# Optimization experiments

Hardware: AMD Instinct MI355X
Metric: run time of the kernel (lower is better)

Reference implementation:

```python
import jax, jax.numpy as jnp
import numpy as np

D_K = 64
N_STEPS = 4
NEG = -1e9  # stand-in for -inf; keeps vjp NaN-free, numerically identical softmax


def setup_inputs() -> dict:
    key = jax.random.key(0)
    ks = jax.random.split(key, 12)
    B, N, D = 4, 2048, 1024
    s = 0.02
    return {
        "hidden": jax.random.normal(ks[0], (B, N, D), jnp.float32),
        "W1": jax.random.normal(ks[1], (64, D), jnp.float32) * s,
        "b1": jnp.zeros((64,), jnp.float32),
        "W2": jax.random.normal(ks[2], (28, 64), jnp.float32) * s,
        "b2": jnp.zeros((28,), jnp.float32),
        "Wq": jax.random.normal(ks[3], (D_K, 28), jnp.float32) * s,
        "Wk": jax.random.normal(ks[4], (D_K, 28), jnp.float32) * s,
        "Wc": jax.random.normal(ks[5], (1, 28), jnp.float32) * s,
        "bc": jnp.zeros((1,), jnp.float32),
        "Wv": jax.random.normal(ks[6], (D_K, D), jnp.float32) * s,
        "Wo": jax.random.normal(ks[7], (D, D_K), jnp.float32) * s,  # torch inits this to zeros; randomized for a non-trivial baseline
        "step_size": jnp.asarray(0.5, jnp.float32),
        "charge_decay": jnp.asarray(0.3, jnp.float32),
        "layer_idx": 0,
    }


def reference(hidden, W1, b1, W2, b2, Wq, Wk, Wc, bc, Wv, Wo, step_size, charge_decay, layer_idx):
    B, N, D = hidden.shape
    # features come from detached hidden in the torch code
    h_sg = jax.lax.stop_gradient(hidden)
    f = jax.nn.gelu(h_sg @ W1.T + b1, approximate=False)  # [B,N,64]
    features = jax.nn.sigmoid(f @ W2.T + b2)              # [B,N,28]
    Q = features @ Wq.T                                   # [B,N,64]
    K = features @ Wk.T                                   # [B,N,64]
    compat = jnp.einsum('bnd,bmd->bnm', Q, K) / jnp.float32(np.sqrt(D_K))
    charge = jax.nn.sigmoid(features @ Wc.T + bc)[..., 0]  # [B,N]
    causal = jnp.tril(jnp.ones((N, N), dtype=bool))
    logits = jnp.where(causal, compat, NEG)
    for _ in range(N_STEPS):
        attn = jax.nn.softmax(logits, axis=-1)            # [B,N,N]
        received = attn.sum(axis=-2)                      # [B,N]
        charge = charge * (1.0 - charge_decay * jax.nn.sigmoid(received - 1.0))
        energy = -compat * charge[:, :, None] * charge[:, None, :]
        logits = jnp.where(causal, logits - step_size * energy, NEG)
    attn = jax.nn.softmax(logits, axis=-1)
    V = hidden @ Wv.T                                     # [B,N,64]
    out = jnp.einsum('bnm,bmd->bnd', attn, V) @ Wo.T      # [B,N,D]
    return out * 0.1
```

## Files before the change

kernel.cpp:

```cpp
#include <hip/hip_runtime.h>
#include <hip/hip_bf16.h>

typedef unsigned short ushort_t;
typedef short bf16x8 __attribute__((ext_vector_type(8)));
typedef ushort_t u16x8 __attribute__((ext_vector_type(8)));
typedef float f32x4 __attribute__((ext_vector_type(4)));

#define DEV static __device__ __forceinline__

DEV float bf2f(ushort_t u) { unsigned v = ((unsigned)u) << 16; float f; __builtin_memcpy(&f, &v, 4); return f; }
DEV short f2bf(float x) { __hip_bfloat16 h = __float2bfloat16(x); short s; __builtin_memcpy(&s, &h, 2); return s; }
DEV float sigm(float x) { return 1.0f / (1.0f + __expf(-x)); }

DEV bf16x8 cvt8(float4 a0, float4 a1) {
    bf16x8 t;
    t[0] = f2bf(a0.x); t[1] = f2bf(a0.y); t[2] = f2bf(a0.z); t[3] = f2bf(a0.w);
    t[4] = f2bf(a1.x); t[5] = f2bf(a1.y); t[6] = f2bf(a1.z); t[7] = f2bf(a1.w);
    return t;
}
DEV bf16x8 ld8f(const float* __restrict__ p) {
    return cvt8(*reinterpret_cast<const float4*>(p), *reinterpret_cast<const float4*>(p + 4));
}

__global__ __launch_bounds__(256, 3) void k_fv(const float* __restrict__ h,
        const float* __restrict__ W1, const float* __restrict__ Wv,
        float* __restrict__ FVp) {
    int bid = blockIdx.x;
    int kh = bid & 1;
    int m0 = (bid >> 1) * 16;
    int wave = threadIdx.x >> 6, lane = threadIdx.x & 63;
    int l16 = lane & 15, quad = lane >> 4;
    const float* B = (wave < 2) ? W1 : Wv;
    int cb = (wave & 1) * 32;
    f32x4 acc[2] = {};
    const float* arow = h + (long)(m0 + l16) * 1024 + kh * 512;
    const float* brow0 = B + (long)(cb + l16) * 1024 + kh * 512;
    const float* brow1 = B + (long)(cb + 16 + l16) * 1024 + kh * 512;
    for (int kc = 0; kc < 512; kc += 128) {
        float4 ra[4][2], r0[4][2], r1[4][2];
#pragma unroll
        for (int u = 0; u < 4; u++) {
            int ko = kc + u * 32 + quad * 8;
            ra[u][0] = *reinterpret_cast<const float4*>(arow + ko);
            ra[u][1] = *reinterpret_cast<const float4*>(arow + ko + 4);
            r0[u][0] = *reinterpret_cast<const float4*>(brow0 + ko);
            r0[u][1] = *reinterpret_cast<const float4*>(brow0 + ko + 4);
            r1[u][0] = *reinterpret_cast<const float4*>(brow1 + ko);
            r1[u][1] = *reinterpret_cast<const float4*>(brow1 + ko + 4);
        }
#pragma unroll
        for (int u = 0; u < 4; u++) {
            bf16x8 af = cvt8(ra[u][0], ra[u][1]);
            bf16x8 b0 = cvt8(r0[u][0], r0[u][1]);
            bf16x8 b1v = cvt8(r1[u][0], r1[u][1]);
            acc[0] = __builtin_amdgcn_mfma_f32_16x16x32_bf16(af, b0, acc[0], 0, 0, 0);
            acc[1] = __builtin_amdgcn_mfma_f32_16x16x32_bf16(af, b1v, acc[1], 0, 0, 0);
        }
    }
    int colbase = ((wave >= 2) ? 64 : 0) + cb;
    float* outp = FVp + (long)kh * 8192 * 128;
#pragma unroll
    for (int c = 0; c < 2; c++)
#pragma unroll
        for (int rr = 0; rr < 4; rr++) {
            int row = m0 + quad * 4 + rr;
            outp[(long)row * 128 + colbase + c * 16 + l16] = acc[c][rr];
        }
}

__global__ __launch_bounds__(256) void k_vbt(const float* __restrict__ FVp, ushort_t* __restrict__ VbT) {
    __shared__ float tL[64][65];
    int r0 = blockIdx.x * 64;
    for (int i = threadIdx.x; i < 64 * 64; i += 256) {
        int r = i >> 6, d = i & 63;
        long idx = (long)(r0 + r) * 128 + 64 + d;
        tL[r][d] = FVp[idx] + FVp[8192L * 128 + idx];
    }
    __syncthreads();
    for (int i = threadIdx.x; i < 64 * 64; i += 256) {
        int d = i >> 6, r = i & 63;
        VbT[(long)d * 8192 + r0 + r] = (ushort_t)f2bf(tL[r][d]);
    }
}

__global__ __launch_bounds__(256) void k_feat(const float* __restrict__ FVp,
        const float* __restrict__ b1, const float* __restrict__ W2, const float* __restrict__ b2,
        const float* __restrict__ Wq, const float* __restrict__ Wk,
        const float* __restrict__ Wc, const float* __restrict__ bc,
        ushort_t* __restrict__ Qb, ushort_t* __restrict__ Kb,
        float* __restrict__ charge0, float* __restrict__ received) {
    __shared__ float w2L[28 * 65], wqL[64 * 29], wkL[64 * 29], wcL[28], b2L[28];
    __shared__ float fL[4][64], featL[4][28];
    int tid = threadIdx.x;
    for (int i = tid; i < 28 * 64; i += 256) w2L[(i >> 6) * 65 + (i & 63)] = W2[i];
    for (int i = tid; i < 64 * 28; i += 256) {
        int r = i / 28, c = i - r * 28;
        wqL[r * 29 + c] = Wq[i];
        wkL[r * 29 + c] = Wk[i];
    }
    if (tid < 28) { wcL[tid] = Wc[tid]; b2L[tid] = b2[tid]; }
    __syncthreads();
    int w = tid >> 6, lane = tid & 63;
    float b1v = b1[lane];
    float bcv = bc[0];
    for (int it = 0; it < 8; it++) {
        int row = blockIdx.x * 32 + it * 4 + w;
        long idx = (long)row * 128 + lane;
        float x = FVp[idx] + FVp[8192L * 128 + idx] + b1v;
        fL[w][lane] = 0.5f * x * (1.0f + erff(x * 0.70710678118654752f));
        __syncthreads();
        if (lane < 28) {
            float s = b2L[lane];
#pragma unroll
            for (int j = 0; j < 64; j++) s += fL[w][j] * w2L[lane * 65 + j];
            featL[w][lane] = sigm(s);
        }
        __syncthreads();
        float q = 0.f, k = 0.f;
#pragma unroll
        for (int i = 0; i < 28; i++) {
            float fv = featL[w][i];
            q += fv * wqL[lane * 29 + i];
            k += fv * wkL[lane * 29 + i];
        }
        Qb[row * 64 + lane] = (ushort_t)f2bf(q * 0.125f);
        Kb[row * 64 + lane] = (ushort_t)f2bf(k);
        if (lane == 0) {
            float c = bcv;
#pragma unroll
            for (int i = 0; i < 28; i++) c += featL[w][i] * wcL[i];
            charge0[row] = sigm(c);
            received[row] = 0.f;
        }
        __syncthreads();
    }
}

DEV void tri_decode(int r, int& ti, int& tj) {
    int t = (int)((sqrtf(8.f * (float)r + 1.f) - 1.f) * 0.5f);
    while ((t + 1) * (t + 2) / 2 <= r) t++;
    while (t * (t + 1) / 2 > r) t--;
    ti = t;
    tj = r - t * (t + 1) / 2;
}

__global__ __launch_bounds__(256) void k_compat(const ushort_t* __restrict__ Qb,
                                                const ushort_t* __restrict__ Kb,
                                                ushort_t* __restrict__ compat) {
    int bid = blockIdx.x;
    int b = bid / 136, r = bid % 136, ti, tj;
    tri_decode(r, ti, tj);
    int wave = threadIdx.x >> 6, lane = threadIdx.x & 63;
    int l16 = lane & 15, quad = lane >> 4;
    int rbase = b * 2048 + ti * 128 + wave * 32;
    int cbase = b * 2048 + tj * 128;
    f32x4 acc[2][8] = {};
#pragma unroll
    for (int kc = 0; kc < 64; kc += 32) {
        int ko = kc + quad * 8;
        bf16x8 af[2], bf[8];
#pragma unroll
        for (int f = 0; f < 2; f++) af[f] = *reinterpret_cast<const bf16x8*>(Qb + (long)(rbase + f * 16 + l16) * 64 + ko);
#pragma unroll
        for (int f = 0; f < 8; f++) bf[f] = *reinterpret_cast<const bf16x8*>(Kb + (long)(cbase + f * 16 + l16) * 64 + ko);
#pragma unroll
        for (int i = 0; i < 2; i++)
#pragma unroll
            for (int j = 0; j < 8; j++)
                acc[i][j] = __builtin_amdgcn_mfma_f32_16x16x32_bf16(af[i], bf[j], acc[i][j], 0, 0, 0);
    }
    int colt = tj * 128;
#pragma unroll
    for (int i = 0; i < 2; i++)
#pragma unroll
        for (int j = 0; j < 8; j++)
#pragma unroll
            for (int rr = 0; rr < 4; rr++) {
                long rowg = rbase + i * 16 + quad * 4 + rr;
                int col = colt + j * 16 + l16;
                compat[rowg * 2048 + col] = (ushort_t)f2bf(acc[i][j][rr]);
            }
}

template <int T>
__global__ __launch_bounds__(256) void k_rowstats(const ushort_t* __restrict__ compat,
        const float4* __restrict__ charges4, const float* __restrict__ stepp,
        float* __restrict__ Lp) {
    int bid = blockIdx.x;
    int z = bid & 1;
    int b = (bid >> 1) & 3;
    int rt = 127 - (bid >> 3);
    int w = threadIdx.x >> 6, lane = threadIdx.x & 63;
    int rw0 = rt * 16 + w * 4;
    int colbase = b * 2048;
    float step = stepp[0];
    float rfx[4] = {}, rfy[4] = {}, rfz[4] = {}, rfw[4] = {};
    if (T > 0) {
#pragma unroll
        for (int r = 0; r < 4; r++) {
            float4 c4 = charges4[colbase + rw0 + r];
            rfx[r] = step * c4.x;
            if (T > 1) rfy[r] = step * c4.y;
            if (T > 2) rfz[r] = step * c4.z;
            if (T > 3) rfw[r] = step * c4.w;
        }
    }
    const ushort_t* crow0 = compat + (long)(colbase + rw0) * 2048;
    float S[4] = {0.f, 0.f, 0.f, 0.f};
    int nmax = rw0 + 3;
    int mhi = min(nmax, z * 1024 + 1023);
    for (int m = z * 1024 + lane; m <= mhi; m += 64) {
        ushort_t cv[4];
#pragma unroll
        for (int r = 0; r < 4; r++) cv[r] = crow0[(long)r * 2048 + m];
        float sx = 0.f, sy = 0.f, sz = 0.f, sw = 0.f;
        if (T > 0) {
            float4 ch = charges4[colbase + m];
            sx = ch.x; sy = ch.y; sz = ch.z; sw = ch.w;
        }
#pragma unroll
        for (int r = 0; r < 4; r++) {
            float sg = 1.f;
            if (T > 0) sg += rfx[r] * sx;
            if (T > 1) sg += rfy[r] * sy;
            if (T > 2) sg += rfz[r] * sz;
            if (T > 3) sg += rfw[r] * sw;
            float e = (m <= rw0 + r) ? __expf(bf2f(cv[r]) * sg) : 0.f;
            S[r] += e;
        }
    }
#pragma unroll
    for (int off = 32; off > 0; off >>= 1) {
#pragma unroll
        for (int r = 0; r < 4; r++) S[r] += __shfl_down(S[r], off);
    }
    if (lane == 0) {
#pragma unroll
        for (int r = 0; r < 4; r++) Lp[z * 8192 + colbase + rw0 + r] = S[r];
    }
}

template <int T>
__global__ __launch_bounds__(256) void k_colsum(const ushort_t* __restrict__ compat,
        const float4* __restrict__ charges4, const float* __restrict__ stepp,
        const float* __restrict__ Lp, float* __restrict__ received) {
    __shared__ float sums[128];
    __shared__ float nvx[32], nvy[32], nvz[32], nvw[32], nLi[32];
    int bid = blockIdx.x;
    int b = bid / 544, rem = bid % 544;
    int q = rem & 3, r = rem >> 2, ti, tj;
    tri_decode(r, ti, tj);
    int tid = threadIdx.x;
    int ml = tid & 127, half = tid >> 7;
    if (tid < 32) {
        int nid = b * 2048 + ti * 128 + q * 32 + tid;
        nLi[tid] = 1.0f / fmaxf(Lp[nid] + Lp[8192 + nid], 1e-30f);
        if (T > 0) {
            float4 cn = charges4[nid];
            nvx[tid] = cn.x;
            if (T > 1) nvy[tid] = cn.y;
            if (T > 2) nvz[tid] = cn.z;
            if (T > 3) nvw[tid] = cn.w;
        }
    }
    __syncthreads();
    int m = tj * 128 + ml;
    int mid = b * 2048 + m;
    float step = stepp[0];
    float cx = 0.f, cy = 0.f, cz = 0.f, cw = 0.f;
    if (T > 0) {
        float4 cm = charges4[mid];
        cx = step * cm.x;
        if (T > 1) cy = step * cm.y;
        if (T > 2) cz = step * cm.z;
        if (T > 3) cw = step * cm.w;
    }
    float acc = 0.f;
    bool diag = (ti == tj);
    const ushort_t* cbase_p = compat + (long)(b * 2048 + ti * 128 + q * 32) * 2048 + m;
    for (int k = 0; k < 16; k += 4) {
        ushort_t cvv[4];
        int nli[4];
#pragma unroll
        for (int u = 0; u < 4; u++) {
            nli[u] = half + 2 * (k + u);
            cvv[u] = cbase_p[(long)nli[u] * 2048];
        }
#pragma unroll
        for (int u = 0; u < 4; u++) {
            float sg = 1.f;
            if (T > 0) sg += cx * nvx[nli[u]];
            if (T > 1) sg += cy * nvy[nli[u]];
            if (T > 2) sg += cz * nvz[nli[u]];
            if (T > 3) sg += cw * nvw[nli[u]];
            float p = __expf(bf2f(cvv[u]) * sg) * nLi[nli[u]];
            if (!diag || m <= ti * 128 + q * 32 + nli[u]) acc += p;
        }
    }
    if (half == 0) sums[ml] = acc;
    __syncthreads();
    if (half == 1) sums[ml] += acc;
    __syncthreads();
    if (tid < 128) atomicAdd(&received[b * 2048 + tj * 128 + tid], sums[tid]);
}

template <int T>
__global__ void k_charge(float* __restrict__ received, const float* __restrict__ charge0,
                         float4* __restrict__ charges4, const float* __restrict__ decayp) {
    int i = blockIdx.x * 256 + threadIdx.x;
    if (i >= 8192) return;
    float decay = decayp[0];
    float rcv = received[i];
    float sg = 1.0f / (1.0f + __expf(1.0f - rcv));
    float prev = (T == 1) ? charge0[i] : ((const float*)&charges4[i])[T - 2];
    ((float*)&charges4[i])[T - 1] = prev * (1.f - decay * sg);
    received[i] = 0.f;
}

__global__ __launch_bounds__(256) void k_pv(const ushort_t* __restrict__ compat,
        const float4* __restrict__ charges4, const float* __restrict__ stepp,
        const ushort_t* __restrict__ VbT, float* __restrict__ Oacc) {
    __shared__ float accL[3][64][17];
    __shared__ float ssL[4][16];
    int bid = blockIdx.x;
    int b = bid & 3, rtile = 127 - (bid >> 2);
    int r0 = rtile * 16;
    int w = threadIdx.x >> 6, lane = threadIdx.x & 63;
    int l16 = lane & 15, quad = lane >> 4;
    int rowl = r0 + l16;
    int rid = b * 2048 + rowl;
    float step = stepp[0];
    float4 c4 = charges4[rid];
    float rx = step * c4.x, ry = step * c4.y, rz = step * c4.z, rw = step * c4.w;
    const ushort_t* crow = compat + (long)rid * 2048;
    f32x4 acc[4] = {};
    float Ss = 0.f;
    int colend = r0 + 16;
    for (int kc = w * 32; kc < colend; kc += 128) {
        int mk = kc + quad * 8;
        u16x8 cv = *reinterpret_cast<const u16x8*>(crow + mk);
        const float4* chp = charges4 + b * 2048 + mk;
        bf16x8 pf;
#pragma unroll
        for (int j = 0; j < 8; j++) {
            float4 ch = chp[j];
            float sg = 1.f + rx * ch.x + ry * ch.y + rz * ch.z + rw * ch.w;
            float p = (mk + j <= rowl) ? __expf(bf2f(cv[j]) * sg) : 0.f;
            Ss += p;
            pf[j] = f2bf(p);
        }
        bf16x8 vf[4];
#pragma unroll
        for (int f = 0; f < 4; f++)
            vf[f] = *reinterpret_cast<const bf16x8*>(VbT + (long)(f * 16 + l16) * 8192 + b * 2048 + mk);
#pragma unroll
        for (int f = 0; f < 4; f++)
            acc[f] = __builtin_amdgcn_mfma_f32_16x16x32_bf16(pf, vf[f], acc[f], 0, 0, 0);
    }
    Ss += __shfl_xor(Ss, 16);
    Ss += __shfl_xor(Ss, 32);
    if (quad == 0) ssL[w][l16] = Ss;
    if (w > 0) {
#pragma unroll
        for (int f = 0; f < 4; f++)
#pragma unroll
            for (int rr = 0; rr < 4; rr++)
                accL[w - 1][lane][f * 4 + rr] = acc[f][rr];
    }
    __syncthreads();
    if (w == 0) {
#pragma unroll
        for (int f = 0; f < 4; f++)
#pragma unroll
            for (int rr = 0; rr < 4; rr++)
                acc[f][rr] += accL[0][lane][f * 4 + rr] + accL[1][lane][f * 4 + rr] + accL[2][lane][f * 4 + rr];
        float Sinv[4];
#pragma unroll
        for (int rr = 0; rr < 4; rr++) {
            int idx = quad * 4 + rr;
            float st = ssL[0][idx] + ssL[1][idx] + ssL[2][idx] + ssL[3][idx];
            Sinv[rr] = 1.f / fmaxf(st, 1e-30f);
        }
#pragma unroll
        for (int f = 0; f < 4; f++)
#pragma unroll
            for (int rr = 0; rr < 4; rr++) {
                int row = r0 + quad * 4 + rr;
                Oacc[(long)(b * 2048 + row) * 64 + f * 16 + l16] = acc[f][rr] * Sinv[rr];
            }
    }
}

__global__ __launch_bounds__(256) void k_oproj(const float* __restrict__ Oacc,
                                               const float* __restrict__ Wo,
                                               float* __restrict__ out) {
    int mt = blockIdx.x & 63, nt = blockIdx.x >> 6;
    int wave = threadIdx.x >> 6, lane = threadIdx.x & 63;
    int wm = wave >> 1, wn = wave & 1;
    int l16 = lane & 15, quad = lane >> 4;
    int row0 = mt * 128 + wm * 64;
    int col0 = nt * 128 + wn * 64;
    f32x4 acc[4][4] = {};
#pragma unroll
    for (int kc = 0; kc < 64; kc += 32) {
        int ko = kc + quad * 8;
        bf16x8 af[4], bfm[4];
#pragma unroll
        for (int f = 0; f < 4; f++) af[f] = ld8f(Oacc + (long)(row0 + f * 16 + l16) * 64 + ko);
#pragma unroll
        for (int f = 0; f < 4; f++) bfm[f] = ld8f(Wo + (long)(col0 + f * 16 + l16) * 64 + ko);
#pragma unroll
        for (int i = 0; i < 4; i++)
#pragma unroll
            for (int j = 0; j < 4; j++)
                acc[i][j] = __builtin_amdgcn_mfma_f32_16x16x32_bf16(af[i], bfm[j], acc[i][j], 0, 0, 0);
    }
#pragma unroll
    for (int i = 0; i < 4; i++)
#pragma unroll
        for (int j = 0; j < 4; j++)
#pragma unroll
            for (int rr = 0; rr < 4; rr++) {
                long rowg = row0 + i * 16 + quad * 4 + rr;
                int colg = col0 + j * 16 + l16;
                out[rowg * 1024 + colg] = acc[i][j][rr] * 0.1f;
            }
}

extern "C" void kernel_launch(void* const* d_in, const int* in_sizes, int n_in,
                              void* d_out, int out_size, void* d_ws, size_t ws_size,
                              hipStream_t stream) {
    const float* hidden = (const float*)d_in[0];
    const float* W1 = (const float*)d_in[1];
    const float* b1 = (const float*)d_in[2];
    const float* W2 = (const float*)d_in[3];
    const float* b2 = (const float*)d_in[4];
    const float* Wq = (const float*)d_in[5];
    const float* Wk = (const float*)d_in[6];
    const float* Wc = (const float*)d_in[7];
    const float* bc = (const float*)d_in[8];
    const float* Wv = (const float*)d_in[9];
    const float* Wo = (const float*)d_in[10];
    const float* stepp = (const float*)d_in[11];
    const float* decayp = (const float*)d_in[12];

    char* ws = (char*)d_ws;
    size_t off = 0;
    auto alloc = [&](size_t bytes) {
        void* p = ws + off;
        off += (bytes + 255) & ~(size_t)255;
        return p;
    };
    ushort_t* compat = (ushort_t*)alloc(8192UL * 2048 * 2);
    float* FVp = (float*)alloc(2UL * 8192 * 128 * 4);
    ushort_t* Qb = (ushort_t*)alloc(8192UL * 64 * 2);
    ushort_t* Kb = (ushort_t*)alloc(8192UL * 64 * 2);
    ushort_t* VbT = (ushort_t*)alloc(64UL * 8192 * 2);
    float* Oacc = (float*)alloc(8192UL * 64 * 4);
    float4* charges4 = (float4*)alloc(8192UL * 16);
    float* charge0 = (float*)alloc(8192UL * 4);
    float* Lp = (float*)alloc(2UL * 8192 * 4);
    float* received = (float*)alloc(8192UL * 4);
    (void)ws_size; (void)in_sizes; (void)n_in; (void)out_size;

    k_fv<<<1024, 256, 0, stream>>>(hidden, W1, Wv, FVp);
    k_vbt<<<128, 256, 0, stream>>>(FVp, VbT);
    k_feat<<<256, 256, 0, stream>>>(FVp, b1, W2, b2, Wq, Wk, Wc, bc, Qb, Kb, charge0, received);
    k_compat<<<544, 256, 0, stream>>>(Qb, Kb, compat);

    k_rowstats<0><<<1024, 256, 0, stream>>>(compat, charges4, stepp, Lp);
    k_colsum<0><<<2176, 256, 0, stream>>>(compat, charges4, stepp, Lp, received);
    k_charge<1><<<32, 256, 0, stream>>>(received, charge0, charges4, decayp);

    k_rowstats<1><<<1024, 256, 0, stream>>>(compat, charges4, stepp, Lp);
    k_colsum<1><<<2176, 256, 0, stream>>>(compat, charges4, stepp, Lp, received);
    k_charge<2><<<32, 256, 0, stream>>>(received, charge0, charges4, decayp);

    k_rowstats<2><<<1024, 256, 0, stream>>>(compat, charges4, stepp, Lp);
    k_colsum<2><<<2176, 256, 0, stream>>>(compat, charges4, stepp, Lp, received);
    k_charge<3><<<32, 256, 0, stream>>>(received, charge0, charges4, decayp);

    k_rowstats<3><<<1024, 256, 0, stream>>>(compat, charges4, stepp, Lp);
    k_colsum<3><<<2176, 256, 0, stream>>>(compat, charges4, stepp, Lp, received);
    k_charge<4><<<32, 256, 0, stream>>>(received, charge0, charges4, decayp);

    k_pv<<<512, 256, 0, stream>>>(compat, charges4, stepp, VbT, Oacc);
    k_oproj<<<512, 256, 0, stream>>>(Oacc, Wo, (float*)d_out);
}
```

Before: 303.5 us.

## Preconvert inputs to bf16, drop split-K in projection, vectorize rowstats/colsum loads

Hidden and the W1/Wv weights are converted to bf16 in a separate pass, and the projection kernel runs full-K without the two-way split. It writes features and the transposed bf16 V directly, which removes the partial-sum buffer and the separate transpose kernel. Row-stats now loads 8 bf16 compat values per lane and exits early for upper-half blocks that lie entirely above the causal diagonal. Column-sum is re-laid out so each thread handles 8 consecutive columns with vector loads and a shared-memory reduction. The cost is an extra conversion pass that reads and writes the full hidden tensor.

```diff
diff --git a/kernel.cpp b/kernel.cpp
--- a/kernel.cpp
+++ b/kernel.cpp
@@ -22,68 +22,54 @@
     return cvt8(*reinterpret_cast<const float4*>(p), *reinterpret_cast<const float4*>(p + 4));
 }
 
-__global__ __launch_bounds__(256, 3) void k_fv(const float* __restrict__ h,
-        const float* __restrict__ W1, const float* __restrict__ Wv,
-        float* __restrict__ FVp) {
-    int bid = blockIdx.x;
-    int kh = bid & 1;
-    int m0 = (bid >> 1) * 16;
+__global__ void k_cvt(const float* __restrict__ src, ushort_t* __restrict__ dst, int n8) {
+    int i = blockIdx.x * 256 + threadIdx.x;
+    if (i >= n8) return;
+    const float4* p = reinterpret_cast<const float4*>(src) + (long)i * 2;
+    *reinterpret_cast<bf16x8*>(dst + (long)i * 8) = cvt8(p[0], p[1]);
+}
+
+__global__ __launch_bounds__(256) void k_fv(const ushort_t* __restrict__ Hb,
+        const ushort_t* __restrict__ Wcat,
+        float* __restrict__ Ff, ushort_t* __restrict__ VbT) {
+    int m0 = blockIdx.x * 16;
     int wave = threadIdx.x >> 6, lane = threadIdx.x & 63;
     int l16 = lane & 15, quad = lane >> 4;
-    const float* B = (wave < 2) ? W1 : Wv;
     int cb = (wave & 1) * 32;
+    int brow_off = (wave < 2) ? 0 : 64;
     f32x4 acc[2] = {};
-    const float* arow = h + (long)(m0 + l16) * 1024 + kh * 512;
-    const float* brow0 = B + (long)(cb + l16) * 1024 + kh * 512;
-    const float* brow1 = B + (long)(cb + 16 + l16) * 1024 + kh * 512;
-    for (int kc = 0; kc < 512; kc += 128) {
-        float4 ra[4][2], r0[4][2], r1[4][2];
+    const ushort_t* arow = Hb + (long)(m0 + l16) * 1024;
+    const ushort_t* brow0 = Wcat + (long)(brow_off + cb + l16) * 1024;
+    const ushort_t* brow1 = Wcat + (long)(brow_off + cb + 16 + l16) * 1024;
+    for (int kc = 0; kc < 1024; kc += 128) {
+        bf16x8 a4[4], b04[4], b14[4];
 #pragma unroll
         for (int u = 0; u < 4; u++) {
             int ko = kc + u * 32 + quad * 8;
-            ra[u][0] = *reinterpret_cast<const float4*>(arow + ko);
-            ra[u][1] = *reinterpret_cast<const float4*>(arow + ko + 4);
-            r0[u][0] = *reinterpret_cast<const float4*>(brow0 + ko);
-            r0[u][1] = *reinterpret_cast<const float4*>(brow0 + ko + 4);
-            r1[u][0] = *reinterpret_cast<const float4*>(brow1 + ko);
-            r1[u][1] = *reinterpret_cast<const float4*>(brow1 + ko + 4);
+            a4[u] = *reinterpret_cast<const bf16x8*>(arow + ko);
+            b04[u] = *reinterpret_cast<const bf16x8*>(brow0 + ko);
+            b14[u] = *reinterpret_cast<const bf16x8*>(brow1 + ko);
         }
 #pragma unroll
         for (int u = 0; u < 4; u++) {
-            bf16x8 af = cvt8(ra[u][0], ra[u][1]);
-            bf16x8 b0 = cvt8(r0[u][0], r0[u][1]);
-            bf16x8 b1v = cvt8(r1[u][0], r1[u][1]);
-            acc[0] = __builtin_amdgcn_mfma_f32_16x16x32_bf16(af, b0, acc[0], 0, 0, 0);
-            acc[1] = __builtin_amdgcn_mfma_f32_16x16x32_bf16(af, b1v, acc[1], 0, 0, 0);
-        }
-    }
-    int colbase = ((wave >= 2) ? 64 : 0) + cb;
-    float* outp = FVp + (long)kh * 8192 * 128;
+            acc[0] = __builtin_amdgcn_mfma_f32_16x16x32_bf16(a4[u], b04[u], acc[0], 0, 0, 0);
+            acc[1] = __builtin_amdgcn_mfma_f32_16x16x32_bf16(a4[u], b14[u], acc[1], 0, 0, 0);
+        }
+    }
+    bool isV = (wave >= 2);
 #pragma unroll
     for (int c = 0; c < 2; c++)
 #pragma unroll
         for (int rr = 0; rr < 4; rr++) {
             int row = m0 + quad * 4 + rr;
-            outp[(long)row * 128 + colbase + c * 16 + l16] = acc[c][rr];
-        }
-}
-
-__global__ __launch_bounds__(256) void k_vbt(const float* __restrict__ FVp, ushort_t* __restrict__ VbT) {
-    __shared__ float tL[64][65];
-    int r0 = blockIdx.x * 64;
-    for (int i = threadIdx.x; i < 64 * 64; i += 256) {
-        int r = i >> 6, d = i & 63;
-        long idx = (long)(r0 + r) * 128 + 64 + d;
-        tL[r][d] = FVp[idx] + FVp[8192L * 128 + idx];
-    }
-    __syncthreads();
-    for (int i = threadIdx.x; i < 64 * 64; i += 256) {
-        int d = i >> 6, r = i & 63;
-        VbT[(long)d * 8192 + r0 + r] = (ushort_t)f2bf(tL[r][d]);
-    }
-}
-
-__global__ __launch_bounds__(256) void k_feat(const float* __restrict__ FVp,
+            int col = cb + c * 16 + l16;
+            float v = acc[c][rr];
+            if (!isV) Ff[row * 64 + col] = v;
+            else VbT[(long)col * 8192 + row] = (ushort_t)f2bf(v);
+        }
+}
+
+__global__ __launch_bounds__(256) void k_feat(const float* __restrict__ Ff,
         const float* __restrict__ b1, const float* __restrict__ W2, const float* __restrict__ b2,
         const float* __restrict__ Wq, const float* __restrict__ Wk,
         const float* __restrict__ Wc, const float* __restrict__ bc,
@@ -105,8 +91,7 @@
     float bcv = bc[0];
     for (int it = 0; it < 8; it++) {
         int row = blockIdx.x * 32 + it * 4 + w;
-        long idx = (long)row * 128 + lane;
-        float x = FVp[idx] + FVp[8192L * 128 + idx] + b1v;
+        float x = Ff[row * 64 + lane] + b1v;
         fL[w][lane] = 0.5f * x * (1.0f + erff(x * 0.70710678118654752f));
         __syncthreads();
         if (lane < 28) {
@@ -193,6 +178,13 @@
     int w = threadIdx.x >> 6, lane = threadIdx.x & 63;
     int rw0 = rt * 16 + w * 4;
     int colbase = b * 2048;
+    if (z == 1 && rt < 64) {
+        if (lane == 0) {
+#pragma unroll
+            for (int r = 0; r < 4; r++) Lp[8192 + colbase + rw0 + r] = 0.f;
+        }
+        return;
+    }
     float step = stepp[0];
     float rfx[4] = {}, rfy[4] = {}, rfz[4] = {}, rfw[4] = {};
     if (T > 0) {
@@ -206,27 +198,32 @@
         }
     }
     const ushort_t* crow0 = compat + (long)(colbase + rw0) * 2048;
+    int nmax = rw0 + 3;
     float S[4] = {0.f, 0.f, 0.f, 0.f};
-    int nmax = rw0 + 3;
-    int mhi = min(nmax, z * 1024 + 1023);
-    for (int m = z * 1024 + lane; m <= mhi; m += 64) {
-        ushort_t cv[4];
-#pragma unroll
-        for (int r = 0; r < 4; r++) cv[r] = crow0[(long)r * 2048 + m];
-        float sx = 0.f, sy = 0.f, sz = 0.f, sw = 0.f;
+#pragma unroll
+    for (int it = 0; it < 2; it++) {
+        int mb = z * 1024 + it * 512 + lane * 8;
+        if (mb > nmax) continue;
+        u16x8 cv[4];
+#pragma unroll
+        for (int r = 0; r < 4; r++) cv[r] = *reinterpret_cast<const u16x8*>(crow0 + (long)r * 2048 + mb);
+        float4 ch[8];
         if (T > 0) {
-            float4 ch = charges4[colbase + m];
-            sx = ch.x; sy = ch.y; sz = ch.z; sw = ch.w;
-        }
-#pragma unroll
-        for (int r = 0; r < 4; r++) {
-            float sg = 1.f;
-            if (T > 0) sg += rfx[r] * sx;
-            if (T > 1) sg += rfy[r] * sy;
-            if (T > 2) sg += rfz[r] * sz;
-            if (T > 3) sg += rfw[r] * sw;
-            float e = (m <= rw0 + r) ? __expf(bf2f(cv[r]) * sg) : 0.f;
-            S[r] += e;
+#pragma unroll
+            for (int j = 0; j < 8; j++) ch[j] = charges4[colbase + mb + j];
+        }
+#pragma unroll
+        for (int j = 0; j < 8; j++) {
+#pragma unroll
+            for (int r = 0; r < 4; r++) {
+                float sg = 1.f;
+                if (T > 0) sg += rfx[r] * ch[j].x;
+                if (T > 1) sg += rfy[r] * ch[j].y;
+                if (T > 2) sg += rfz[r] * ch[j].z;
+                if (T > 3) sg += rfw[r] * ch[j].w;
+                float e = (mb + j <= rw0 + r) ? __expf(bf2f(cv[r][j]) * sg) : 0.f;
+                S[r] += e;
+            }
         }
     }
 #pragma unroll
@@ -244,64 +241,73 @@
 __global__ __launch_bounds__(256) void k_colsum(const ushort_t* __restrict__ compat,
         const float4* __restrict__ charges4, const float* __restrict__ stepp,
         const float* __restrict__ Lp, float* __restrict__ received) {
-    __shared__ float sums[128];
     __shared__ float nvx[32], nvy[32], nvz[32], nvw[32], nLi[32];
+    __shared__ float sums[16][136];
     int bid = blockIdx.x;
     int b = bid / 544, rem = bid % 544;
     int q = rem & 3, r = rem >> 2, ti, tj;
     tri_decode(r, ti, tj);
     int tid = threadIdx.x;
-    int ml = tid & 127, half = tid >> 7;
+    float step = stepp[0];
     if (tid < 32) {
         int nid = b * 2048 + ti * 128 + q * 32 + tid;
         nLi[tid] = 1.0f / fmaxf(Lp[nid] + Lp[8192 + nid], 1e-30f);
         if (T > 0) {
             float4 cn = charges4[nid];
-            nvx[tid] = cn.x;
-            if (T > 1) nvy[tid] = cn.y;
-            if (T > 2) nvz[tid] = cn.z;
-            if (T > 3) nvw[tid] = cn.w;
+            nvx[tid] = step * cn.x;
+            if (T > 1) nvy[tid] = step * cn.y;
+            if (T > 2) nvz[tid] = step * cn.z;
+            if (T > 3) nvw[tid] = step * cn.w;
         }
     }
     __syncthreads();
-    int m = tj * 128 + ml;
-    int mid = b * 2048 + m;
-    float step = stepp[0];
-    float cx = 0.f, cy = 0.f, cz = 0.f, cw = 0.f;
+    int cg = tid & 15, ng = tid >> 4;
+    int m0 = tj * 128 + cg * 8;
+    long mid0 = (long)b * 2048 + m0;
+    float4 cm[8];
     if (T > 0) {
-        float4 cm = charges4[mid];
-        cx = step * cm.x;
-        if (T > 1) cy = step * cm.y;
-        if (T > 2) cz = step * cm.z;
-        if (T > 3) cw = step * cm.w;
-    }
-    float acc = 0.f;
+#pragma unroll
+        for (int j = 0; j < 8; j++) cm[j] = charges4[mid0 + j];
+    }
     bool diag = (ti == tj);
-    const ushort_t* cbase_p = compat + (long)(b * 2048 + ti * 128 + q * 32) * 2048 + m;
-    for (int k = 0; k < 16; k += 4) {
-        ushort_t cvv[4];
-        int nli[4];
-#pragma unroll
-        for (int u = 0; u < 4; u++) {
-            nli[u] = half + 2 * (k + u);
-            cvv[u] = cbase_p[(long)nli[u] * 2048];
-        }
-#pragma unroll
-        for (int u = 0; u < 4; u++) {
+    u16x8 cva[2];
+    int nla[2];
+#pragma unroll
+    for (int t2 = 0; t2 < 2; t2++) {
+        nla[t2] = q * 32 + ng + t2 * 16;
+        long nid = (long)b * 2048 + ti * 128 + nla[t2];
+        cva[t2] = *reinterpret_cast<const u16x8*>(compat + nid * 2048 + m0);
+    }
+    float acc[8] = {};
+#pragma unroll
+    for (int t2 = 0; t2 < 2; t2++) {
+        int nloc = ng + t2 * 16;
+        float Li = nLi[nloc];
+        float ax = (T > 0) ? nvx[nloc] : 0.f;
+        float ay = (T > 1) ? nvy[nloc] : 0.f;
+        float az = (T > 2) ? nvz[nloc] : 0.f;
+        float aw = (T > 3) ? nvw[nloc] : 0.f;
+        int nglob = ti * 128 + nla[t2];
+#pragma unroll
+        for (int j = 0; j < 8; j++) {
             float sg = 1.f;
-            if (T > 0) sg += cx * nvx[nli[u]];
-            if (T > 1) sg += cy * nvy[nli[u]];
-            if (T > 2) sg += cz * nvz[nli[u]];
-            if (T > 3) sg += cw * nvw[nli[u]];
-            float p = __expf(bf2f(cvv[u]) * sg) * nLi[nli[u]];
-            if (!diag || m <= ti * 128 + q * 32 + nli[u]) acc += p;
-        }
-    }
-    if (half == 0) sums[ml] = acc;
+            if (T > 0) sg += ax * cm[j].x;
+            if (T > 1) sg += ay * cm[j].y;
+            if (T > 2) sg += az * cm[j].z;
+            if (T > 3) sg += aw * cm[j].w;
+            float p = __expf(bf2f(cva[t2][j]) * sg) * Li;
+            if (!diag || m0 + j <= nglob) acc[j] += p;
+        }
+    }
+#pragma unroll
+    for (int j = 0; j < 8; j++) sums[ng][cg * 8 + j] = acc[j];
     __syncthreads();
-    if (half == 1) sums[ml] += acc;
-    __syncthreads();
-    if (tid < 128) atomicAdd(&received[b * 2048 + tj * 128 + tid], sums[tid]);
+    if (tid < 128) {
+        float s = 0.f;
+#pragma unroll
+        for (int g = 0; g < 16; g++) s += sums[g][tid];
+        atomicAdd(&received[b * 2048 + tj * 128 + tid], s);
+    }
 }
 
 template <int T>
@@ -452,7 +458,9 @@
         return p;
     };
     ushort_t* compat = (ushort_t*)alloc(8192UL * 2048 * 2);
-    float* FVp = (float*)alloc(2UL * 8192 * 128 * 4);
+    ushort_t* Hb = (ushort_t*)alloc(8192UL * 1024 * 2);
+    ushort_t* Wcat = (ushort_t*)alloc(128UL * 1024 * 2);
+    float* Ff = (float*)alloc(8192UL * 64 * 4);
     ushort_t* Qb = (ushort_t*)alloc(8192UL * 64 * 2);
     ushort_t* Kb = (ushort_t*)alloc(8192UL * 64 * 2);
     ushort_t* VbT = (ushort_t*)alloc(64UL * 8192 * 2);
@@ -463,9 +471,11 @@
     float* received = (float*)alloc(8192UL * 4);
     (void)ws_size; (void)in_sizes; (void)n_in; (void)out_size;
 
-    k_fv<<<1024, 256, 0, stream>>>(hidden, W1, Wv, FVp);
-    k_vbt<<<128, 256, 0, stream>>>(FVp, VbT);
-    k_feat<<<256, 256, 0, stream>>>(FVp, b1, W2, b2, Wq, Wk, Wc, bc, Qb, Kb, charge0, received);
+    k_cvt<<<4096, 256, 0, stream>>>(hidden, Hb, 8192 * 1024 / 8);
+    k_cvt<<<32, 256, 0, stream>>>(W1, Wcat, 64 * 1024 / 8);
+    k_cvt<<<32, 256, 0, stream>>>(Wv, Wcat + 64 * 1024, 64 * 1024 / 8);
+    k_fv<<<512, 256, 0, stream>>>(Hb, Wcat, Ff, VbT);
+    k_feat<<<256, 256, 0, stream>>>(Ff, b1, W2, b2, Wq, Wk, Wc, bc, Qb, Kb, charge0, received);
     k_compat<<<544, 256, 0, stream>>>(Qb, Kb, compat);
 
     k_rowstats<0><<<1024, 256, 0, stream>>>(compat, charges4, stepp, Lp);
```

Measured after the change: 291.9 us. 3.8% less time.
